# Optimization experiments

Hardware: AMD Instinct MI355X
Metric: run time of the kernel (lower is better)

The kernel has to match this reference:

```python
import jax, jax.numpy as jnp
import numpy as np

WS = 7            # window size
DISP = WS // 2    # cyclic displacement = 3
HEADS = 8
HD = 32           # head dims = skip_channels // num_heads
NEG = -jnp.inf

def _rel_indices(ws):
    idx = np.array([[i // ws, i % ws] for i in range(ws * ws)], dtype=np.int64)
    rel = idx[None, :, :] - idx[:, None, :] + ws - 1  # (ws^2, ws^2, 2)
    return rel

def _masks(ws, d):
    n = ws * ws
    ul = np.zeros((n, n), dtype=np.float32)
    ul[-d * ws:, :-d * ws] = -np.inf
    ul[:-d * ws, -d * ws:] = -np.inf
    lr = np.zeros((ws, ws, ws, ws), dtype=np.float32)
    lr[:, -d:, :, :-d] = -np.inf
    lr[:, :-d, :, -d:] = -np.inf
    return ul, lr.reshape(n, n)

REL = _rel_indices(WS)                 # np (49,49,2)
UL_MASK, LR_MASK = _masks(WS, DISP)    # np (49,49) each


def setup_inputs() -> dict:
    key = jax.random.key(0)
    ks = jax.random.split(key, 7)
    B, C, H, W = 16, 256, 56, 56
    scale = 1.0 / np.sqrt(HD)
    return {
        "skip": jax.random.normal(ks[0], (B, H * W, C), jnp.float32),
        "x": jax.random.normal(ks[1], (B, H * W, C), jnp.float32),
        "Wq": jax.random.normal(ks[2], (HD, HD), jnp.float32) * scale,
        "Wk": jax.random.normal(ks[3], (HD, HD), jnp.float32) * scale,
        "Wv": jax.random.normal(ks[4], (HD, HD), jnp.float32) * scale,
        "Wl": jax.random.normal(ks[5], (HD, HD), jnp.float32) * scale,
        "pe": jax.random.normal(ks[6], (2 * WS - 1, 2 * WS - 1), jnp.float32),
        "b": B, "c": C, "h": H, "w": W,
    }


def _forward(skip, x, Wq, Wk, Wv, Wl, pe, b, c, h, w):
    # tokens -> images (B,C,H,W)
    xi = x.transpose(0, 2, 1).reshape(b, c, h, w)
    si = skip.transpose(0, 2, 1).reshape(b, c, h, w)
    # cyclic shift (propagate with -disp)
    xi = jnp.roll(xi, (-DISP, -DISP), axis=(2, 3))
    si = jnp.roll(si, (-DISP, -DISP), axis=(2, 3))
    n_h, n_w = h // WS, w // WS
    ws2 = WS * WS

    def to_windows(t):
        t = t.reshape(b, HEADS, HD, n_h, WS, n_w, WS)
        t = t.transpose(0, 1, 3, 5, 4, 6, 2)
        return t.reshape(b, HEADS, n_h * n_w, ws2, HD)

    xw = to_windows(xi)   # (B,H,nW,ws2,hd)
    sw = to_windows(si)
    q = xw @ Wq.T
    k = xw @ Wk.T
    v = sw @ Wv.T
    qk = jnp.einsum('bhnqd,bhnkd->bhnqk', q, k) / np.sqrt(HD)
    bias = pe[REL[:, :, 0], REL[:, :, 1]]          # (ws2, ws2)
    qk = qk + bias[None, None, None]
    qk = qk.at[:, :, -n_w:].add(jnp.asarray(UL_MASK))
    qk = qk.at[:, :, n_w - 1::n_w].add(jnp.asarray(LR_MASK))
    attn = jax.nn.softmax(qk, axis=-1)
    out = jnp.einsum('bhnqk,bhnkd->bhnqd', attn, v) @ Wl.T
    # windows -> image
    out = out.transpose(0, 1, 4, 2, 3).reshape(b, c, n_h, n_w, WS, WS)
    out = out.transpose(0, 1, 2, 4, 3, 5).reshape(b, c, h, w)
    out = jnp.roll(out, (DISP, DISP), axis=(2, 3))  # revert shift
    return out.reshape(b, c, h * w).transpose(0, 2, 1)


def reference(skip, x, Wq, Wk, Wv, Wl, pe, b, c, h, w):
    return _forward(skip, x, Wq, Wk, Wv, Wl, pe, b, c, h, w)
```

## Files before the change

### kernel.cpp

```cpp
#include <hip/hip_runtime.h>
#include <math.h>

#define WS    7
#define WS2   49
#define DISP  3
#define HEADS 8
#define HD    32
#define IMGH  56
#define IMGW  56

typedef __attribute__((ext_vector_type(8))) __bf16 bf16x8;
typedef __attribute__((ext_vector_type(8))) short short8;
typedef __attribute__((ext_vector_type(4))) short short4v;
typedef __attribute__((ext_vector_type(4))) float f32x4;

__device__ __forceinline__ short f2bf(float f) {
  unsigned u = __builtin_bit_cast(unsigned, f);
  unsigned r = (u + 0x7fffu + ((u >> 16) & 1u)) >> 16;
  return (short)r;
}
__device__ __forceinline__ float bf2f(short s) {
  unsigned u = ((unsigned)(unsigned short)s) << 16;
  return __builtin_bit_cast(float, u);
}

__global__ void prep_kernel(const float* __restrict__ Wq, const float* __restrict__ Wk,
                            const float* __restrict__ Wv, const float* __restrict__ Wl,
                            const float* __restrict__ pe, short* __restrict__ wsW,
                            short* __restrict__ wsB) {
  __shared__ float lw[4096];
  __shared__ float lpe[176];
  const int t = threadIdx.x;
  const int gid = blockIdx.x * 256 + t;
  for (int i = t; i < 1024; i += 256) {
    lw[i] = Wq[i]; lw[1024 + i] = Wk[i]; lw[2048 + i] = Wv[i]; lw[3072 + i] = Wl[i];
  }
  if (t < 169) lpe[t] = pe[t];
  __syncthreads();
  if (gid < 1024) {
    int k = gid >> 5, n = gid & 31; float acc = 0.f;
    #pragma unroll
    for (int d = 0; d < 32; d++) acc += lw[d * 32 + k] * lw[1024 + d * 32 + n];
    wsW[n * 40 + k] = f2bf(acc * 0.17677669529663687f);
  } else if (gid < 2048) {
    int e = gid - 1024; int m = e >> 5, n = e & 31; float acc = 0.f;
    #pragma unroll
    for (int d = 0; d < 32; d++) acc += lw[3072 + m * 32 + d] * lw[2048 + d * 32 + n];
    wsW[1280 + m * 40 + n] = f2bf(acc);
  }
  for (int e = gid; e < 13328; e += 4096) {
    int v = e / 3332, r2 = e % 3332, q = r2 / 68, k = r2 % 68;
    float val;
    if (k >= 49) val = -INFINITY;
    else {
      int qy = q / 7, qx = q % 7, ky = k / 7, kx = k % 7;
      bool masked = ((v & 2) && ((qy >= 4) != (ky >= 4))) ||
                    ((v & 1) && ((qx >= 4) != (kx >= 4)));
      val = masked ? -INFINITY : lpe[(ky - qy + 6) * 13 + (kx - qx + 6)];
    }
    wsB[e] = f2bf(val);
  }
}

__global__ __launch_bounds__(256, 2) void swca_kernel(
    const float* __restrict__ skip, const float* __restrict__ x,
    const short* __restrict__ wsW, const short* __restrict__ wsB,
    float* __restrict__ out) {
  __shared__ __align__(16) char smem[64272];
  short* biasb = (short*)smem;
  short* wqkt  = (short*)(smem + 6672);
  short* w2r   = (short*)(smem + 9232);
  int*   gaddr = (int*)(smem + 11792);
  char*  arena = smem + 12048;

  const int t = threadIdx.x, blk = blockIdx.x;
  const int win = blk & 63, b = blk >> 6, wy = win >> 3, wx = win & 7;

  {
    int v = ((wy == 7) ? 2 : 0) | ((wx == 7) ? 1 : 0);
    const int* bs = (const int*)(wsB + v * 3332);
    int* bd = (int*)biasb;
    for (int i = t; i < 1666; i += 256) bd[i] = bs[i];
    const int* wsrc = (const int*)wsW;
    int* wdst = (int*)wqkt;
    for (int i = t; i < 1280; i += 256) wdst[i] = wsrc[i];
    if (t < 64) {
      int p = t, ga = 0;
      if (p < 49) {
        int py = p / 7, px = p % 7;
        int r = (wy * 7 + py + DISP) % IMGH, c = (wx * 7 + px + DISP) % IMGW;
        ga = (b * 3136 + r * 56 + c) * 256;
      }
      gaddr[t] = ga;
    }
  }
  __syncthreads();

  const int w = t >> 6, l = t & 63;
  const int lrow = l & 15, g = l >> 4, lk8 = g * 8;
  short* Tb = (short*)(arena + w * 13056);
  short* Pb = (short*)(arena + w * 13056);
  short* UT = (short*)(arena + w * 13056 + 8704);
  const f32x4 zero = {0.f, 0.f, 0.f, 0.f};

  for (int hh = 0; hh < 2; hh++) {
    const int h = w * 2 + hh;
    bf16x8 ax[4], asf[4];
    #pragma unroll
    for (int tm = 0; tm < 4; tm++) {
      short8 sa = {0,0,0,0,0,0,0,0}, ss = {0,0,0,0,0,0,0,0};
      int p = tm * 16 + lrow;
      if (p < 49) {
        int ga = gaddr[p] + h * 32 + lk8;
        float4 x0 = *(const float4*)(x + ga);
        float4 x1 = *(const float4*)(x + ga + 4);
        float4 s0 = *(const float4*)(skip + ga);
        float4 s1 = *(const float4*)(skip + ga + 4);
        sa[0]=f2bf(x0.x); sa[1]=f2bf(x0.y); sa[2]=f2bf(x0.z); sa[3]=f2bf(x0.w);
        sa[4]=f2bf(x1.x); sa[5]=f2bf(x1.y); sa[6]=f2bf(x1.z); sa[7]=f2bf(x1.w);
        ss[0]=f2bf(s0.x); ss[1]=f2bf(s0.y); ss[2]=f2bf(s0.z); ss[3]=f2bf(s0.w);
        ss[4]=f2bf(s1.x); ss[5]=f2bf(s1.y); ss[6]=f2bf(s1.z); ss[7]=f2bf(s1.w);
      }
      ax[tm]  = __builtin_bit_cast(bf16x8, sa);
      asf[tm] = __builtin_bit_cast(bf16x8, ss);
    }
    bf16x8 bq[2], bw[2];
    #pragma unroll
    for (int tn = 0; tn < 2; tn++) {
      int n = tn * 16 + lrow;
      bq[tn] = *(const bf16x8*)(wqkt + n * 40 + lk8);
      bw[tn] = *(const bf16x8*)(w2r  + n * 40 + lk8);
    }
    #pragma unroll
    for (int tm = 0; tm < 4; tm++) {
      int row0 = tm * 16 + g * 4;
      #pragma unroll
      for (int tn = 0; tn < 2; tn++) {
        int col = tn * 16 + lrow;
        f32x4 tD = __builtin_amdgcn_mfma_f32_16x16x32_bf16(ax[tm], bq[tn], zero, 0, 0, 0);
        Tb[(row0 + 0) * 36 + col] = f2bf(tD[0]);
        Tb[(row0 + 1) * 36 + col] = f2bf(tD[1]);
        Tb[(row0 + 2) * 36 + col] = f2bf(tD[2]);
        Tb[(row0 + 3) * 36 + col] = f2bf(tD[3]);
        f32x4 uD = __builtin_amdgcn_mfma_f32_16x16x32_bf16(asf[tm], bw[tn], zero, 0, 0, 0);
        short4v u4 = { f2bf(uD[0]), f2bf(uD[1]), f2bf(uD[2]), f2bf(uD[3]) };
        *(short4v*)(UT + col * 68 + row0) = u4;
      }
    }
    bf16x8 bT[4];
    #pragma unroll
    for (int tn = 0; tn < 4; tn++) {
      int n = tn * 16 + lrow;
      short4v lo = *(const short4v*)(Tb + n * 36 + lk8);
      short4v hi = *(const short4v*)(Tb + n * 36 + lk8 + 4);
      short8 c; c[0]=lo[0];c[1]=lo[1];c[2]=lo[2];c[3]=lo[3];
                c[4]=hi[0];c[5]=hi[1];c[6]=hi[2];c[7]=hi[3];
      bT[tn] = __builtin_bit_cast(bf16x8, c);
    }
    f32x4 st[4][4];
    #pragma unroll
    for (int ti = 0; ti < 4; ti++)
      #pragma unroll
      for (int tj = 0; tj < 4; tj++)
        st[ti][tj] = __builtin_amdgcn_mfma_f32_16x16x32_bf16(ax[ti], bT[tj], zero, 0, 0, 0);
    #pragma unroll
    for (int tj = 0; tj < 4; tj++) {
      int q = tj * 16 + lrow;
      int qc = q > 48 ? 48 : q;
      float vv[4][4]; float mx = -INFINITY;
      #pragma unroll
      for (int ti = 0; ti < 4; ti++) {
        int k0 = ti * 16 + g * 4;
        short4v b4 = *(const short4v*)(biasb + qc * 68 + k0);
        vv[ti][0] = st[ti][tj][0] + bf2f(b4[0]);
        vv[ti][1] = st[ti][tj][1] + bf2f(b4[1]);
        vv[ti][2] = st[ti][tj][2] + bf2f(b4[2]);
        vv[ti][3] = st[ti][tj][3] + bf2f(b4[3]);
        mx = fmaxf(mx, fmaxf(fmaxf(vv[ti][0], vv[ti][1]), fmaxf(vv[ti][2], vv[ti][3])));
      }
      mx = fmaxf(mx, __shfl_xor(mx, 16));
      mx = fmaxf(mx, __shfl_xor(mx, 32));
      float sum = 0.f;
      #pragma unroll
      for (int ti = 0; ti < 4; ti++) {
        vv[ti][0] = __expf(vv[ti][0] - mx); sum += vv[ti][0];
        vv[ti][1] = __expf(vv[ti][1] - mx); sum += vv[ti][1];
        vv[ti][2] = __expf(vv[ti][2] - mx); sum += vv[ti][2];
        vv[ti][3] = __expf(vv[ti][3] - mx); sum += vv[ti][3];
      }
      sum += __shfl_xor(sum, 16);
      sum += __shfl_xor(sum, 32);
      float inv = 1.f / sum;
      #pragma unroll
      for (int ti = 0; ti < 4; ti++) {
        int k0 = ti * 16 + g * 4;
        short4v p4 = { f2bf(vv[ti][0] * inv), f2bf(vv[ti][1] * inv),
                       f2bf(vv[ti][2] * inv), f2bf(vv[ti][3] * inv) };
        *(short4v*)(Pb + q * 68 + k0) = p4;
      }
    }
    f32x4 oD[4][2];
    #pragma unroll
    for (int tr = 0; tr < 4; tr++)
      #pragma unroll
      for (int tn = 0; tn < 2; tn++) oD[tr][tn] = zero;
    #pragma unroll
    for (int ks = 0; ks < 2; ks++) {
      int kof = ks * 32 + lk8;
      bf16x8 aP[4], bU[2];
      #pragma unroll
      for (int tr = 0; tr < 4; tr++) {
        int q = tr * 16 + lrow;
        short4v lo = *(const short4v*)(Pb + q * 68 + kof);
        short4v hi = *(const short4v*)(Pb + q * 68 + kof + 4);
        short8 c; c[0]=lo[0];c[1]=lo[1];c[2]=lo[2];c[3]=lo[3];
                  c[4]=hi[0];c[5]=hi[1];c[6]=hi[2];c[7]=hi[3];
        aP[tr] = __builtin_bit_cast(bf16x8, c);
      }
      #pragma unroll
      for (int tn = 0; tn < 2; tn++) {
        int n = tn * 16 + lrow;
        short4v lo = *(const short4v*)(UT + n * 68 + kof);
        short4v hi = *(const short4v*)(UT + n * 68 + kof + 4);
        short8 c; c[0]=lo[0];c[1]=lo[1];c[2]=lo[2];c[3]=lo[3];
                  c[4]=hi[0];c[5]=hi[1];c[6]=hi[2];c[7]=hi[3];
        bU[tn] = __builtin_bit_cast(bf16x8, c);
      }
      #pragma unroll
      for (int tr = 0; tr < 4; tr++)
        #pragma unroll
        for (int tn = 0; tn < 2; tn++)
          oD[tr][tn] = __builtin_amdgcn_mfma_f32_16x16x32_bf16(aP[tr], bU[tn], oD[tr][tn], 0, 0, 0);
    }
    #pragma unroll
    for (int tr = 0; tr < 4; tr++) {
      int p0 = tr * 16 + g * 4;
      #pragma unroll
      for (int r = 0; r < 4; r++) {
        int p = p0 + r;
        if (p < 49) {
          int ga = gaddr[p] + h * 32;
          out[ga + lrow]      = oD[tr][0][r];
          out[ga + 16 + lrow] = oD[tr][1][r];
        }
      }
    }
  }
}

extern "C" void kernel_launch(void* const* d_in, const int* in_sizes, int n_in,
                              void* d_out, int out_size, void* d_ws, size_t ws_size,
                              hipStream_t stream) {
  const float* skip = (const float*)d_in[0];
  const float* x    = (const float*)d_in[1];
  const float* Wq   = (const float*)d_in[2];
  const float* Wk   = (const float*)d_in[3];
  const float* Wv   = (const float*)d_in[4];
  const float* Wl   = (const float*)d_in[5];
  const float* pe   = (const float*)d_in[6];
  float* out = (float*)d_out;
  short* wsW = (short*)d_ws;
  short* wsB = wsW + 2560;

  prep_kernel<<<16, 256, 0, stream>>>(Wq, Wk, Wv, Wl, pe, wsW, wsB);
  swca_kernel<<<16 * 64, 256, 0, stream>>>(skip, x, wsW, wsB, out);
}
```

Baseline: 175.6 us.

## Keep bias in registers, shrink LDS, hoist loads, raise occupancy to three blocks

The attention bias tile moves from shared memory into per-thread registers and the per-wave arena shrinks, cutting LDS so three blocks can fit per CU (launch bounds raised to 3). Global loads for both heads are hoisted ahead of compute to expose more memory parallelism. QK^T is computed one column tile at a time inside the softmax loop to reduce live accumulators, and manual bf16 rounding is replaced with native __bf16 conversions. Holding the bias and both heads' inputs in registers raises register pressure and may cause spills under the tighter launch bound.

```diff
diff --git a/kernel.cpp b/kernel.cpp
--- a/kernel.cpp
+++ b/kernel.cpp
@@ -1,16 +1,12 @@
 #include <hip/hip_runtime.h>
 #include <math.h>
 
-#define WS    7
-#define WS2   49
 #define DISP  3
-#define HEADS 8
-#define HD    32
 #define IMGH  56
 #define IMGW  56
 
 typedef __attribute__((ext_vector_type(8))) __bf16 bf16x8;
-typedef __attribute__((ext_vector_type(8))) short short8;
+typedef __attribute__((ext_vector_type(4))) __bf16 bf16x4;
 typedef __attribute__((ext_vector_type(4))) short short4v;
 typedef __attribute__((ext_vector_type(4))) float f32x4;
 
@@ -62,27 +58,37 @@
   }
 }
 
-__global__ __launch_bounds__(256, 2) void swca_kernel(
+__global__ __launch_bounds__(256, 3) void swca_kernel(
     const float* __restrict__ skip, const float* __restrict__ x,
     const short* __restrict__ wsW, const short* __restrict__ wsB,
     float* __restrict__ out) {
-  __shared__ __align__(16) char smem[64272];
-  short* biasb = (short*)smem;
-  short* wqkt  = (short*)(smem + 6672);
-  short* w2r   = (short*)(smem + 9232);
-  int*   gaddr = (int*)(smem + 11792);
-  char*  arena = smem + 12048;
+  __shared__ __align__(16) char smem[49472];
+  __bf16* wqkt  = (__bf16*)smem;
+  __bf16* w2r   = (__bf16*)(smem + 2560);
+  int*    gaddr = (int*)(smem + 5120);
+  char*   arena = smem + 5376;
 
   const int t = threadIdx.x, blk = blockIdx.x;
   const int win = blk & 63, b = blk >> 6, wy = win >> 3, wx = win & 7;
-
+  const int w = t >> 6, l = t & 63;
+  const int lrow = l & 15, g = l >> 4, lk8 = g * 8;
+
+  short4v bias[4][4];
   {
     int v = ((wy == 7) ? 2 : 0) | ((wx == 7) ? 1 : 0);
-    const int* bs = (const int*)(wsB + v * 3332);
-    int* bd = (int*)biasb;
-    for (int i = t; i < 1666; i += 256) bd[i] = bs[i];
+    const short* bb = wsB + v * 3332;
+    #pragma unroll
+    for (int tj = 0; tj < 4; tj++) {
+      int q = tj * 16 + lrow; int qc = q > 48 ? 48 : q;
+      #pragma unroll
+      for (int ti = 0; ti < 4; ti++)
+        bias[tj][ti] = *(const short4v*)(bb + qc * 68 + ti * 16 + g * 4);
+    }
+  }
+
+  {
     const int* wsrc = (const int*)wsW;
-    int* wdst = (int*)wqkt;
+    int* wdst = (int*)smem;
     for (int i = t; i < 1280; i += 256) wdst[i] = wsrc[i];
     if (t < 64) {
       int p = t, ga = 0;
@@ -96,19 +102,19 @@
   }
   __syncthreads();
 
-  const int w = t >> 6, l = t & 63;
-  const int lrow = l & 15, g = l >> 4, lk8 = g * 8;
-  short* Tb = (short*)(arena + w * 13056);
-  short* Pb = (short*)(arena + w * 13056);
-  short* UT = (short*)(arena + w * 13056 + 8704);
-  const f32x4 zero = {0.f, 0.f, 0.f, 0.f};
-
+  __bf16* Tb = (__bf16*)(arena + w * 11024);
+  __bf16* Pb = Tb;
+  __bf16* UT = (__bf16*)(arena + w * 11024 + 6672);
+
+  bf16x8 axh[2][4], ash[2][4];
+  #pragma unroll
   for (int hh = 0; hh < 2; hh++) {
     const int h = w * 2 + hh;
-    bf16x8 ax[4], asf[4];
     #pragma unroll
     for (int tm = 0; tm < 4; tm++) {
-      short8 sa = {0,0,0,0,0,0,0,0}, ss = {0,0,0,0,0,0,0,0};
+      bf16x8 a, s;
+      #pragma unroll
+      for (int j = 0; j < 8; j++) { a[j] = (__bf16)0.0f; s[j] = (__bf16)0.0f; }
       int p = tm * 16 + lrow;
       if (p < 49) {
         int ga = gaddr[p] + h * 32 + lk8;
@@ -116,14 +122,20 @@
         float4 x1 = *(const float4*)(x + ga + 4);
         float4 s0 = *(const float4*)(skip + ga);
         float4 s1 = *(const float4*)(skip + ga + 4);
-        sa[0]=f2bf(x0.x); sa[1]=f2bf(x0.y); sa[2]=f2bf(x0.z); sa[3]=f2bf(x0.w);
-        sa[4]=f2bf(x1.x); sa[5]=f2bf(x1.y); sa[6]=f2bf(x1.z); sa[7]=f2bf(x1.w);
-        ss[0]=f2bf(s0.x); ss[1]=f2bf(s0.y); ss[2]=f2bf(s0.z); ss[3]=f2bf(s0.w);
-        ss[4]=f2bf(s1.x); ss[5]=f2bf(s1.y); ss[6]=f2bf(s1.z); ss[7]=f2bf(s1.w);
-      }
-      ax[tm]  = __builtin_bit_cast(bf16x8, sa);
-      asf[tm] = __builtin_bit_cast(bf16x8, ss);
-    }
+        a[0]=(__bf16)x0.x; a[1]=(__bf16)x0.y; a[2]=(__bf16)x0.z; a[3]=(__bf16)x0.w;
+        a[4]=(__bf16)x1.x; a[5]=(__bf16)x1.y; a[6]=(__bf16)x1.z; a[7]=(__bf16)x1.w;
+        s[0]=(__bf16)s0.x; s[1]=(__bf16)s0.y; s[2]=(__bf16)s0.z; s[3]=(__bf16)s0.w;
+        s[4]=(__bf16)s1.x; s[5]=(__bf16)s1.y; s[6]=(__bf16)s1.z; s[7]=(__bf16)s1.w;
+      }
+      axh[hh][tm] = a; ash[hh][tm] = s;
+    }
+  }
+
+  const f32x4 zero = {0.f, 0.f, 0.f, 0.f};
+
+  #pragma unroll
+  for (int hh = 0; hh < 2; hh++) {
+    const int h = w * 2 + hh;
     bf16x8 bq[2], bw[2];
     #pragma unroll
     for (int tn = 0; tn < 2; tn++) {
@@ -137,45 +149,38 @@
       #pragma unroll
       for (int tn = 0; tn < 2; tn++) {
         int col = tn * 16 + lrow;
-        f32x4 tD = __builtin_amdgcn_mfma_f32_16x16x32_bf16(ax[tm], bq[tn], zero, 0, 0, 0);
-        Tb[(row0 + 0) * 36 + col] = f2bf(tD[0]);
-        Tb[(row0 + 1) * 36 + col] = f2bf(tD[1]);
-        Tb[(row0 + 2) * 36 + col] = f2bf(tD[2]);
-        Tb[(row0 + 3) * 36 + col] = f2bf(tD[3]);
-        f32x4 uD = __builtin_amdgcn_mfma_f32_16x16x32_bf16(asf[tm], bw[tn], zero, 0, 0, 0);
-        short4v u4 = { f2bf(uD[0]), f2bf(uD[1]), f2bf(uD[2]), f2bf(uD[3]) };
-        *(short4v*)(UT + col * 68 + row0) = u4;
+        f32x4 tD = __builtin_amdgcn_mfma_f32_16x16x32_bf16(axh[hh][tm], bq[tn], zero, 0, 0, 0);
+        Tb[(row0 + 0) * 36 + col] = (__bf16)tD[0];
+        Tb[(row0 + 1) * 36 + col] = (__bf16)tD[1];
+        Tb[(row0 + 2) * 36 + col] = (__bf16)tD[2];
+        Tb[(row0 + 3) * 36 + col] = (__bf16)tD[3];
+        f32x4 uD = __builtin_amdgcn_mfma_f32_16x16x32_bf16(ash[hh][tm], bw[tn], zero, 0, 0, 0);
+        bf16x4 u4 = {(__bf16)uD[0], (__bf16)uD[1], (__bf16)uD[2], (__bf16)uD[3]};
+        *(bf16x4*)(UT + col * 68 + row0) = u4;
       }
     }
     bf16x8 bT[4];
     #pragma unroll
     for (int tn = 0; tn < 4; tn++) {
       int n = tn * 16 + lrow;
-      short4v lo = *(const short4v*)(Tb + n * 36 + lk8);
-      short4v hi = *(const short4v*)(Tb + n * 36 + lk8 + 4);
-      short8 c; c[0]=lo[0];c[1]=lo[1];c[2]=lo[2];c[3]=lo[3];
-                c[4]=hi[0];c[5]=hi[1];c[6]=hi[2];c[7]=hi[3];
-      bT[tn] = __builtin_bit_cast(bf16x8, c);
-    }
-    f32x4 st[4][4];
-    #pragma unroll
-    for (int ti = 0; ti < 4; ti++)
-      #pragma unroll
-      for (int tj = 0; tj < 4; tj++)
-        st[ti][tj] = __builtin_amdgcn_mfma_f32_16x16x32_bf16(ax[ti], bT[tj], zero, 0, 0, 0);
+      bf16x4 lo = *(const bf16x4*)(Tb + n * 36 + lk8);
+      bf16x4 hi = *(const bf16x4*)(Tb + n * 36 + lk8 + 4);
+      bT[tn] = __builtin_shufflevector(lo, hi, 0, 1, 2, 3, 4, 5, 6, 7);
+    }
     #pragma unroll
     for (int tj = 0; tj < 4; tj++) {
+      f32x4 stj[4];
+      #pragma unroll
+      for (int ti = 0; ti < 4; ti++)
+        stj[ti] = __builtin_amdgcn_mfma_f32_16x16x32_bf16(axh[hh][ti], bT[tj], zero, 0, 0, 0);
       int q = tj * 16 + lrow;
-      int qc = q > 48 ? 48 : q;
       float vv[4][4]; float mx = -INFINITY;
       #pragma unroll
       for (int ti = 0; ti < 4; ti++) {
-        int k0 = ti * 16 + g * 4;
-        short4v b4 = *(const short4v*)(biasb + qc * 68 + k0);
-        vv[ti][0] = st[ti][tj][0] + bf2f(b4[0]);
-        vv[ti][1] = st[ti][tj][1] + bf2f(b4[1]);
-        vv[ti][2] = st[ti][tj][2] + bf2f(b4[2]);
-        vv[ti][3] = st[ti][tj][3] + bf2f(b4[3]);
+        vv[ti][0] = stj[ti][0] + bf2f(bias[tj][ti][0]);
+        vv[ti][1] = stj[ti][1] + bf2f(bias[tj][ti][1]);
+        vv[ti][2] = stj[ti][2] + bf2f(bias[tj][ti][2]);
+        vv[ti][3] = stj[ti][3] + bf2f(bias[tj][ti][3]);
         mx = fmaxf(mx, fmaxf(fmaxf(vv[ti][0], vv[ti][1]), fmaxf(vv[ti][2], vv[ti][3])));
       }
       mx = fmaxf(mx, __shfl_xor(mx, 16));
@@ -191,12 +196,13 @@
       sum += __shfl_xor(sum, 16);
       sum += __shfl_xor(sum, 32);
       float inv = 1.f / sum;
-      #pragma unroll
-      for (int ti = 0; ti < 4; ti++) {
-        int k0 = ti * 16 + g * 4;
-        short4v p4 = { f2bf(vv[ti][0] * inv), f2bf(vv[ti][1] * inv),
-                       f2bf(vv[ti][2] * inv), f2bf(vv[ti][3] * inv) };
-        *(short4v*)(Pb + q * 68 + k0) = p4;
+      if (q < 49) {
+        #pragma unroll
+        for (int ti = 0; ti < 4; ti++) {
+          bf16x4 p4 = {(__bf16)(vv[ti][0] * inv), (__bf16)(vv[ti][1] * inv),
+                       (__bf16)(vv[ti][2] * inv), (__bf16)(vv[ti][3] * inv)};
+          *(bf16x4*)(Pb + q * 68 + ti * 16 + g * 4) = p4;
+        }
       }
     }
     f32x4 oD[4][2];
@@ -211,20 +217,16 @@
       #pragma unroll
       for (int tr = 0; tr < 4; tr++) {
         int q = tr * 16 + lrow;
-        short4v lo = *(const short4v*)(Pb + q * 68 + kof);
-        short4v hi = *(const short4v*)(Pb + q * 68 + kof + 4);
-        short8 c; c[0]=lo[0];c[1]=lo[1];c[2]=lo[2];c[3]=lo[3];
-                  c[4]=hi[0];c[5]=hi[1];c[6]=hi[2];c[7]=hi[3];
-        aP[tr] = __builtin_bit_cast(bf16x8, c);
+        bf16x4 lo = *(const bf16x4*)(Pb + q * 68 + kof);
+        bf16x4 hi = *(const bf16x4*)(Pb + q * 68 + kof + 4);
+        aP[tr] = __builtin_shufflevector(lo, hi, 0, 1, 2, 3, 4, 5, 6, 7);
       }
       #pragma unroll
       for (int tn = 0; tn < 2; tn++) {
         int n = tn * 16 + lrow;
-        short4v lo = *(const short4v*)(UT + n * 68 + kof);
-        short4v hi = *(const short4v*)(UT + n * 68 + kof + 4);
-        short8 c; c[0]=lo[0];c[1]=lo[1];c[2]=lo[2];c[3]=lo[3];
-                  c[4]=hi[0];c[5]=hi[1];c[6]=hi[2];c[7]=hi[3];
-        bU[tn] = __builtin_bit_cast(bf16x8, c);
+        bf16x4 lo = *(const bf16x4*)(UT + n * 68 + kof);
+        bf16x4 hi = *(const bf16x4*)(UT + n * 68 + kof + 4);
+        bU[tn] = __builtin_shufflevector(lo, hi, 0, 1, 2, 3, 4, 5, 6, 7);
       }
       #pragma unroll
       for (int tr = 0; tr < 4; tr++)
```

Measured after the change: 198.8 us. +13.2%, slower.
